# Optimization experiments

Measured on AMD Instinct MI355X. Metric: run time of the kernel, lower is better.

## Reference

```python
import jax, jax.numpy as jnp
import numpy as np

N_NODES = 20000
N_EDGES = 320000
IN_FEATS = 256
H_FEATS = 256


def setup_inputs() -> dict:
    key = jax.random.key(0)
    ks = jax.random.split(key, 8)
    s = 1.0 / np.sqrt(IN_FEATS)
    return {
        "features": jax.random.normal(ks[0], (N_NODES, IN_FEATS), jnp.float32),
        "src": jax.random.randint(ks[1], (N_EDGES,), 0, N_NODES, jnp.int32),
        "dst": jax.random.randint(ks[2], (N_EDGES,), 0, N_NODES, jnp.int32),
        "W_self1": jax.random.normal(ks[3], (IN_FEATS, H_FEATS), jnp.float32) * s,
        "W_neigh1": jax.random.normal(ks[4], (IN_FEATS, H_FEATS), jnp.float32) * s,
        "b1": jnp.zeros((H_FEATS,), jnp.float32),
        "W_self2": jax.random.normal(ks[5], (H_FEATS, H_FEATS), jnp.float32) * s,
        "W_neigh2": jax.random.normal(ks[6], (H_FEATS, H_FEATS), jnp.float32) * s,
        "b2": jnp.zeros((H_FEATS,), jnp.float32),
    }


def _sage_conv(h, src, dst, W_self, W_neigh, b, n_nodes):
    # mean aggregation of src features onto dst nodes (DGL SAGEConv 'mean')
    msg_sum = jax.ops.segment_sum(h[src], dst, num_segments=n_nodes)  # [N, d]
    deg = jax.ops.segment_sum(jnp.ones_like(dst, dtype=h.dtype), dst,
                              num_segments=n_nodes)  # [N]
    h_neigh = msg_sum / jnp.maximum(deg, 1.0)[:, None]  # isolated nodes -> 0
    return h @ W_self + h_neigh @ W_neigh + b


def reference(features, src, dst, W_self1, W_neigh1, b1, W_self2, W_neigh2, b2):
    n = features.shape[0]
    h = _sage_conv(features, src, dst, W_self1, W_neigh1, b1, n)
    h = jax.nn.relu(h)
    h = _sage_conv(h, src, dst, W_self2, W_neigh2, b2, n)
    # DotPredictor: per-edge dot product of src/dst embeddings
    score = jnp.sum(h[src] * h[dst], axis=1)  # [E]
    return score
```

## Files before the change

### kernel.cpp

```cpp
#include <hip/hip_runtime.h>
#include <hip/hip_bf16.h>
#include <stdint.h>

typedef __bf16 bf16_t;
typedef __bf16 bf16x8 __attribute__((ext_vector_type(8)));
typedef __bf16 bf16x4 __attribute__((ext_vector_type(4)));
typedef float f32x4 __attribute__((ext_vector_type(4)));

#define NFEAT 256
#define KDIM  512
#define BM 64
#define BN 128
#define BK 64

__device__ __forceinline__ void gload_lds16(const void* g, void* l) {
  __builtin_amdgcn_global_load_lds(
      (const __attribute__((address_space(1))) unsigned int*)g,
      (__attribute__((address_space(3))) unsigned int*)l, 16, 0, 0);
}


__global__ void k_count_deg(const int* __restrict__ dst, int* __restrict__ deg, int nE) {
  int i = blockIdx.x * blockDim.x + threadIdx.x;
  if (i < nE) atomicAdd(&deg[dst[i]], 1);
}

__global__ __launch_bounds__(256) void k_scan_part(const int* __restrict__ deg,
                                                   int* __restrict__ partial, int n) {
  const int tid = threadIdx.x;
  int i = blockIdx.x * 256 + tid;
  int d = (i < n) ? deg[i] : 0;
  #pragma unroll
  for (int off = 32; off; off >>= 1) d += __shfl_xor(d, off, 64);
  __shared__ int ws[4];
  if ((tid & 63) == 0) ws[tid >> 6] = d;
  __syncthreads();
  if (tid == 0) partial[blockIdx.x] = ws[0] + ws[1] + ws[2] + ws[3];
}

__global__ __launch_bounds__(256) void k_scan_final(const int* __restrict__ deg,
                                                    const int* __restrict__ partial,
                                                    int* __restrict__ offsets,
                                                    int* __restrict__ cursor,
                                                    float* __restrict__ inv_deg,
                                                    int n, int nb) {
  __shared__ int s[256], p[256];
  const int tid = threadIdx.x;
  int pv = (tid < nb) ? partial[tid] : 0;
  p[tid] = pv;
  __syncthreads();
  for (int off = 1; off < 256; off <<= 1) {
    int v = (tid >= off) ? p[tid - off] : 0;
    __syncthreads();
    p[tid] += v;
    __syncthreads();
  }
  int i = blockIdx.x * 256 + tid;
  int d = (i < n) ? deg[i] : 0;
  s[tid] = d;
  __syncthreads();
  for (int off = 1; off < 256; off <<= 1) {
    int v = (tid >= off) ? s[tid - off] : 0;
    __syncthreads();
    s[tid] += v;
    __syncthreads();
  }
  if (i < n) {
    int block_excl = p[blockIdx.x] - partial[blockIdx.x];
    int excl = block_excl + s[tid] - d;
    offsets[i] = excl;
    cursor[i]  = excl;
    inv_deg[i] = 1.0f / (float)(d > 1 ? d : 1);
  }
}

__global__ void k_scatter(const int* __restrict__ src, const int* __restrict__ dst,
                          int* __restrict__ cursor, int4* __restrict__ csr_pack, int nE) {
  int i = blockIdx.x * blockDim.x + threadIdx.x;
  if (i < nE) {
    int d = dst[i];
    int pos = atomicAdd(&cursor[d], 1);
    csr_pack[pos] = make_int4(src[i], d, i, 0);
  }
}

__global__ void k_prep(const float* __restrict__ F,
                       const float* __restrict__ Ws1, const float* __restrict__ Wn1,
                       const float* __restrict__ Ws2, const float* __restrict__ Wn2,
                       bf16_t* __restrict__ WT1, bf16_t* __restrict__ WT2,
                       bf16_t* __restrict__ X,
                       int* __restrict__ deg, int nNodes, int mpad) {
  int t = blockIdx.x * blockDim.x + threadIdx.x;
  if (t < mpad) deg[t] = 0;
  if (t < 2 * NFEAT * KDIM) {
    int layer = t >> 17;
    int r = t & (NFEAT * KDIM - 1);
    int n = r >> 9;
    int k = r & 511;
    const float* Ws = layer ? Ws2 : Ws1;
    const float* Wn = layer ? Wn2 : Wn1;
    float v = (k < NFEAT) ? Ws[k * NFEAT + n] : Wn[(k - NFEAT) * NFEAT + n];
    (layer ? WT2 : WT1)[r] = (bf16_t)v;
  }
  int n = t >> 6;
  int c = (t & 63) * 4;
  if (n < mpad) {
    float4 v = make_float4(0.f, 0.f, 0.f, 0.f);
    if (n < nNodes) v = *(const float4*)&F[(size_t)n * NFEAT + c];
    bf16x4 o;
    o[0] = (bf16_t)v.x; o[1] = (bf16_t)v.y; o[2] = (bf16_t)v.z; o[3] = (bf16_t)v.w;
    *(bf16x4*)&X[(size_t)n * KDIM + c] = o;
  }
}

__global__ __launch_bounds__(256) void k_agg(const bf16_t* __restrict__ Hin,
                                             bf16_t* __restrict__ Hout,
                                             const int4* __restrict__ csr_pack,
                                             const int* __restrict__ offsets,
                                             const int* __restrict__ deg,
                                             const float* __restrict__ inv_deg,
                                             int instride, int outstride) {
  const int n   = blockIdx.x * 8 + (threadIdx.x >> 5);
  const int l32 = threadIdx.x & 31;
  const int beg = offsets[n];
  const int cnt = deg[n];
  const size_t colo = (size_t)l32 * 8;

  float acc[8] = {0.f, 0.f, 0.f, 0.f, 0.f, 0.f, 0.f, 0.f};

  int s[4];
  #pragma unroll
  for (int q = 0; q < 4; ++q) s[q] = (q < cnt) ? csr_pack[beg + q].x : -1;

  for (int i = 0; i < cnt; i += 4) {
    bf16x8 v[4];
    bool h[4];
    #pragma unroll
    for (int q = 0; q < 4; ++q) {
      h[q] = (s[q] >= 0);
      if (h[q]) v[q] = *(const bf16x8*)&Hin[(size_t)s[q] * instride + colo];
    }
    #pragma unroll
    for (int q = 0; q < 4; ++q) {
      int j = i + 4 + q;
      s[q] = (j < cnt) ? csr_pack[beg + j].x : -1;
    }
    #pragma unroll
    for (int q = 0; q < 4; ++q) {
      if (h[q]) {
        #pragma unroll
        for (int e = 0; e < 8; ++e) acc[e] += (float)v[q][e];
      }
    }
  }

  float w = inv_deg[n];
  bf16x8 o;
  #pragma unroll
  for (int e = 0; e < 8; ++e) o[e] = (bf16_t)(acc[e] * w);
  *(bf16x8*)&Hout[(size_t)n * outstride + NFEAT + colo] = o;
}

__global__ __launch_bounds__(256, 3) void k_gemm(const bf16_t* __restrict__ A,
                                                 const bf16_t* __restrict__ BT,
                                                 const float* __restrict__ bias,
                                                 bf16_t* __restrict__ Cout,
                                                 int ostride, int relu) {
  __shared__ __align__(16) bf16_t As[2][BM * BK];
  __shared__ __align__(16) bf16_t Bs[2][BN * BK];
  const int tid  = threadIdx.x;
  const int lane = tid & 63;
  const int wave = tid >> 6;
  const int wr = wave >> 1, wc = wave & 1;
  const int m0 = blockIdx.x * BM;
  const int n0 = blockIdx.y * BN;
  const int l15 = lane & 15;
  const int lk8 = (lane >> 4) * 8;

  f32x4 acc[2][4] = {};

  auto stage = [&](int buf, int kt) {
    const int k0 = kt * BK;
    #pragma unroll
    for (int i = 0; i < 2; ++i) {
      int idx = i * 256 + tid;
      int row = idx >> 3;
      int c8  = (idx & 7) * 8;
      gload_lds16(A + (size_t)(m0 + row) * KDIM + k0 + c8,
                  (char*)&As[buf][0] + (i * 256 + wave * 64) * 16);
    }
    #pragma unroll
    for (int i = 0; i < 4; ++i) {
      int idx = i * 256 + tid;
      int row = idx >> 3;
      int c8  = (idx & 7) * 8;
      gload_lds16(BT + (size_t)(n0 + row) * KDIM + k0 + c8,
                  (char*)&Bs[buf][0] + (i * 256 + wave * 64) * 16);
    }
  };

  auto compute = [&](int buf) {
    #pragma unroll
    for (int kk = 0; kk < 2; ++kk) {
      bf16x8 af[2], bfr[4];
      #pragma unroll
      for (int m = 0; m < 2; ++m) {
        int row = wr * 32 + m * 16 + l15;
        af[m] = *(const bf16x8*)&As[buf][row * BK + kk * 32 + lk8];
      }
      #pragma unroll
      for (int n = 0; n < 4; ++n) {
        int col = wc * 64 + n * 16 + l15;
        bfr[n] = *(const bf16x8*)&Bs[buf][col * BK + kk * 32 + lk8];
      }
      #pragma unroll
      for (int m = 0; m < 2; ++m)
        #pragma unroll
        for (int n = 0; n < 4; ++n)
          acc[m][n] = __builtin_amdgcn_mfma_f32_16x16x32_bf16(af[m], bfr[n], acc[m][n], 0, 0, 0);
    }
  };

  stage(0, 0);
  __syncthreads();
  const int nt = KDIM / BK;
  int cur = 0;
  for (int t = 0; t < nt; ++t) {
    if (t + 1 < nt) stage(cur ^ 1, t + 1);
    compute(cur);
    __syncthreads();
    cur ^= 1;
  }

  #pragma unroll
  for (int n = 0; n < 4; ++n) {
    int col = n0 + wc * 64 + n * 16 + l15;
    float bv = bias[col];
    #pragma unroll
    for (int m = 0; m < 2; ++m) {
      int rbase = m0 + wr * 32 + m * 16 + (lane >> 4) * 4;
      #pragma unroll
      for (int j = 0; j < 4; ++j) {
        float v = acc[m][n][j] + bv;
        if (relu) v = fmaxf(v, 0.f);
        Cout[(size_t)(rbase + j) * ostride + col] = (bf16_t)v;
      }
    }
  }
}

__global__ __launch_bounds__(256) void k_edge_dot(const bf16_t* __restrict__ H,
                                                  const int4* __restrict__ csr_pack,
                                                  float* __restrict__ out, int nE) {
  const int wid  = (blockIdx.x * blockDim.x + threadIdx.x) >> 6;
  const int lane = threadIdx.x & 63;
  const int l15  = lane & 15;
  const int hi   = lane >> 4;
  const int e0   = wid * 16;
  if (e0 >= nE) return;
  int pos = e0 + l15;
  if (pos >= nE) pos = nE - 1;

  const int4 e = csr_pack[pos];
  const bf16_t* ps = H + (size_t)e.x * NFEAT + hi * 8;
  const bf16_t* pd = H + (size_t)e.y * NFEAT + hi * 8;

  f32x4 acc = {0.f, 0.f, 0.f, 0.f};
  #pragma unroll
  for (int ks = 0; ks < 8; ++ks) {
    bf16x8 a = *(const bf16x8*)(ps + ks * 32);
    bf16x8 b = *(const bf16x8*)(pd + ks * 32);
    acc = __builtin_amdgcn_mfma_f32_16x16x32_bf16(a, b, acc, 0, 0, 0);
  }

  if ((l15 >> 2) == hi && (e0 + l15) < nE) {
    int j = l15 & 3;
    float v = acc[0];
    v = (j == 1) ? acc[1] : v;
    v = (j == 2) ? acc[2] : v;
    v = (j == 3) ? acc[3] : v;
    out[e.z] = v;
  }
}


extern "C" void kernel_launch(void* const* d_in, const int* in_sizes, int n_in,
                              void* d_out, int out_size, void* d_ws, size_t ws_size,
                              hipStream_t stream) {
  const float* features = (const float*)d_in[0];
  const int*   src      = (const int*)d_in[1];
  const int*   dst      = (const int*)d_in[2];
  const float* Wself1   = (const float*)d_in[3];
  const float* Wneigh1  = (const float*)d_in[4];
  const float* b1       = (const float*)d_in[5];
  const float* Wself2   = (const float*)d_in[6];
  const float* Wneigh2  = (const float*)d_in[7];
  const float* b2       = (const float*)d_in[8];
  float* score = (float*)d_out;

  const int nNodes = in_sizes[0] / NFEAT;
  const int nE     = in_sizes[1];
  const int mpad   = ((nNodes + 127) / 128) * 128;

  char* ws = (char*)d_ws;
  size_t off = 0;
  auto alloc = [&](size_t bytes) { char* p = ws + off; off += (bytes + 255) & ~(size_t)255; return p; };
  bf16_t* Xcat1   = (bf16_t*)alloc((size_t)mpad * KDIM * 2);
  bf16_t* Xcat2   = (bf16_t*)alloc((size_t)mpad * KDIM * 2);
  bf16_t* H2      = (bf16_t*)alloc((size_t)mpad * NFEAT * 2);
  bf16_t* WT1     = (bf16_t*)alloc((size_t)NFEAT * KDIM * 2);
  bf16_t* WT2     = (bf16_t*)alloc((size_t)NFEAT * KDIM * 2);
  int*    deg     = (int*)alloc((size_t)mpad * 4);
  int*    offsets = (int*)alloc((size_t)mpad * 4);
  int*    cursor  = (int*)alloc((size_t)mpad * 4);
  float*  inv_deg = (float*)alloc((size_t)mpad * 4);
  int4*   csr_pack= (int4*)alloc((size_t)nE * 16);
  int*    partial = (int*)alloc(1024 * 4);

  const int eb = (nE + 255) / 256;
  const int nb = (mpad + 255) / 256;

  k_prep<<<(mpad * 64 + 255) / 256, 256, 0, stream>>>(features, Wself1, Wneigh1,
                                                      Wself2, Wneigh2, WT1, WT2,
                                                      Xcat1, deg, nNodes, mpad);

  k_count_deg<<<eb, 256, 0, stream>>>(dst, deg, nE);
  k_scan_part<<<nb, 256, 0, stream>>>(deg, partial, mpad);
  k_scan_final<<<nb, 256, 0, stream>>>(deg, partial, offsets, cursor, inv_deg, mpad, nb);
  k_scatter<<<eb, 256, 0, stream>>>(src, dst, cursor, csr_pack, nE);

  k_agg<<<mpad / 8, 256, 0, stream>>>(Xcat1, Xcat1, csr_pack, offsets, deg, inv_deg, KDIM, KDIM);
  dim3 ggrid(mpad / BM, NFEAT / BN);
  k_gemm<<<ggrid, 256, 0, stream>>>(Xcat1, WT1, b1, Xcat2, KDIM, 1);

  k_agg<<<mpad / 8, 256, 0, stream>>>(Xcat2, Xcat2, csr_pack, offsets, deg, inv_deg, KDIM, KDIM);
  k_gemm<<<ggrid, 256, 0, stream>>>(Xcat2, WT2, b2, H2, NFEAT, 0);

  const int nWaves = (nE + 15) / 16;
  k_edge_dot<<<(nWaves + 3) / 4, 256, 0, stream>>>(H2, csr_pack, score, nE);
}
```

Baseline: 152.1 us.

## Fuse neighbor aggregation into GEMM, single-pass scan, and compact CSR edge packing

Mean aggregation now runs inside the GEMM kernel. Each block gathers neighbor rows for its 64 nodes into a swizzled LDS tile and uses that tile as the second half of K, so the aggregated features no longer go through global memory and the separate agg launches are dropped. The GEMM tile widens to the full 256 output columns with 512 threads. The two scan kernels become one decoupled-lookback scan that spins on global flags and resets them for the next call. The CSR pack shrinks from int4 to a src array plus an int2 holding 16-bit-packed src/dst and the edge id. The 16-bit packing assumes fewer than 65536 nodes, the spin-wait relies on all blocks making forward progress, and the fused kernel needs much more LDS, which may lower occupancy.

```diff
diff --git a/kernel.cpp b/kernel.cpp
--- a/kernel.cpp
+++ b/kernel.cpp
@@ -10,7 +10,7 @@
 #define NFEAT 256
 #define KDIM  512
 #define BM 64
-#define BN 128
+#define BN 256
 #define BK 64
 
 __device__ __forceinline__ void gload_lds16(const void* g, void* l) {
@@ -19,43 +19,25 @@
       (__attribute__((address_space(3))) unsigned int*)l, 16, 0, 0);
 }
 
+__device__ int g_flag[256];
+__device__ int g_depart;
+
 
 __global__ void k_count_deg(const int* __restrict__ dst, int* __restrict__ deg, int nE) {
   int i = blockIdx.x * blockDim.x + threadIdx.x;
   if (i < nE) atomicAdd(&deg[dst[i]], 1);
 }
 
-__global__ __launch_bounds__(256) void k_scan_part(const int* __restrict__ deg,
-                                                   int* __restrict__ partial, int n) {
-  const int tid = threadIdx.x;
-  int i = blockIdx.x * 256 + tid;
-  int d = (i < n) ? deg[i] : 0;
-  #pragma unroll
-  for (int off = 32; off; off >>= 1) d += __shfl_xor(d, off, 64);
-  __shared__ int ws[4];
-  if ((tid & 63) == 0) ws[tid >> 6] = d;
-  __syncthreads();
-  if (tid == 0) partial[blockIdx.x] = ws[0] + ws[1] + ws[2] + ws[3];
-}
-
-__global__ __launch_bounds__(256) void k_scan_final(const int* __restrict__ deg,
-                                                    const int* __restrict__ partial,
+__global__ __launch_bounds__(256) void k_scan_fused(const int* __restrict__ deg,
                                                     int* __restrict__ offsets,
                                                     int* __restrict__ cursor,
                                                     float* __restrict__ inv_deg,
                                                     int n, int nb) {
-  __shared__ int s[256], p[256];
+  __shared__ int s[256];
+  __shared__ int p[256];
+  const int b = blockIdx.x;
   const int tid = threadIdx.x;
-  int pv = (tid < nb) ? partial[tid] : 0;
-  p[tid] = pv;
-  __syncthreads();
-  for (int off = 1; off < 256; off <<= 1) {
-    int v = (tid >= off) ? p[tid - off] : 0;
-    __syncthreads();
-    p[tid] += v;
-    __syncthreads();
-  }
-  int i = blockIdx.x * 256 + tid;
+  int i = b * 256 + tid;
   int d = (i < n) ? deg[i] : 0;
   s[tid] = d;
   __syncthreads();
@@ -65,22 +47,46 @@
     s[tid] += v;
     __syncthreads();
   }
+  if (tid == 255) atomicExch(&g_flag[b], s[255] + 1);
+  int pv = 0;
+  if (tid < b) {
+    int v;
+    do { v = atomicAdd(&g_flag[tid], 0); } while (v == 0);
+    pv = v - 1;
+  }
+  p[tid] = pv;
+  __syncthreads();
+  for (int off = 128; off; off >>= 1) {
+    if (tid < off) p[tid] += p[tid + off];
+    __syncthreads();
+  }
+  int block_excl = p[0];
   if (i < n) {
-    int block_excl = p[blockIdx.x] - partial[blockIdx.x];
     int excl = block_excl + s[tid] - d;
     offsets[i] = excl;
     cursor[i]  = excl;
     inv_deg[i] = 1.0f / (float)(d > 1 ? d : 1);
   }
+  __syncthreads();
+  if (tid == 0) {
+    int old = atomicAdd(&g_depart, 1);
+    if (old == nb - 1) {
+      for (int j = 0; j < nb; ++j) atomicExch(&g_flag[j], 0);
+      atomicExch(&g_depart, 0);
+    }
+  }
 }
 
 __global__ void k_scatter(const int* __restrict__ src, const int* __restrict__ dst,
-                          int* __restrict__ cursor, int4* __restrict__ csr_pack, int nE) {
+                          int* __restrict__ cursor, int* __restrict__ csr_src,
+                          int2* __restrict__ epack, int nE) {
   int i = blockIdx.x * blockDim.x + threadIdx.x;
   if (i < nE) {
     int d = dst[i];
+    int s = src[i];
     int pos = atomicAdd(&cursor[d], 1);
-    csr_pack[pos] = make_int4(src[i], d, i, 0);
+    csr_src[pos] = s;
+    epack[pos] = make_int2((d << 16) | s, i);
   }
 }
 
@@ -109,148 +115,152 @@
     if (n < nNodes) v = *(const float4*)&F[(size_t)n * NFEAT + c];
     bf16x4 o;
     o[0] = (bf16_t)v.x; o[1] = (bf16_t)v.y; o[2] = (bf16_t)v.z; o[3] = (bf16_t)v.w;
-    *(bf16x4*)&X[(size_t)n * KDIM + c] = o;
-  }
-}
-
-__global__ __launch_bounds__(256) void k_agg(const bf16_t* __restrict__ Hin,
-                                             bf16_t* __restrict__ Hout,
-                                             const int4* __restrict__ csr_pack,
-                                             const int* __restrict__ offsets,
-                                             const int* __restrict__ deg,
-                                             const float* __restrict__ inv_deg,
-                                             int instride, int outstride) {
-  const int n   = blockIdx.x * 8 + (threadIdx.x >> 5);
-  const int l32 = threadIdx.x & 31;
-  const int beg = offsets[n];
-  const int cnt = deg[n];
-  const size_t colo = (size_t)l32 * 8;
-
-  float acc[8] = {0.f, 0.f, 0.f, 0.f, 0.f, 0.f, 0.f, 0.f};
-
-  int s[4];
-  #pragma unroll
-  for (int q = 0; q < 4; ++q) s[q] = (q < cnt) ? csr_pack[beg + q].x : -1;
-
-  for (int i = 0; i < cnt; i += 4) {
-    bf16x8 v[4];
-    bool h[4];
-    #pragma unroll
-    for (int q = 0; q < 4; ++q) {
-      h[q] = (s[q] >= 0);
-      if (h[q]) v[q] = *(const bf16x8*)&Hin[(size_t)s[q] * instride + colo];
-    }
-    #pragma unroll
-    for (int q = 0; q < 4; ++q) {
-      int j = i + 4 + q;
-      s[q] = (j < cnt) ? csr_pack[beg + j].x : -1;
-    }
-    #pragma unroll
-    for (int q = 0; q < 4; ++q) {
-      if (h[q]) {
-        #pragma unroll
-        for (int e = 0; e < 8; ++e) acc[e] += (float)v[q][e];
-      }
-    }
-  }
-
-  float w = inv_deg[n];
-  bf16x8 o;
-  #pragma unroll
-  for (int e = 0; e < 8; ++e) o[e] = (bf16_t)(acc[e] * w);
-  *(bf16x8*)&Hout[(size_t)n * outstride + NFEAT + colo] = o;
-}
-
-__global__ __launch_bounds__(256, 3) void k_gemm(const bf16_t* __restrict__ A,
-                                                 const bf16_t* __restrict__ BT,
-                                                 const float* __restrict__ bias,
-                                                 bf16_t* __restrict__ Cout,
-                                                 int ostride, int relu) {
+    *(bf16x4*)&X[(size_t)n * NFEAT + c] = o;
+  }
+}
+
+__global__ __launch_bounds__(512, 2) void k_gemm_agg(
+    const bf16_t* __restrict__ Xin,
+    const bf16_t* __restrict__ BT,
+    const float*  __restrict__ bias,
+    bf16_t* __restrict__ Cout,
+    const int* __restrict__ csr_src,
+    const int* __restrict__ offsets,
+    const int* __restrict__ deg,
+    const float* __restrict__ inv_deg,
+    int relu) {
   __shared__ __align__(16) bf16_t As[2][BM * BK];
   __shared__ __align__(16) bf16_t Bs[2][BN * BK];
+  __shared__ __align__(16) bf16_t Ag[BM * 256];
   const int tid  = threadIdx.x;
   const int lane = tid & 63;
   const int wave = tid >> 6;
-  const int wr = wave >> 1, wc = wave & 1;
-  const int m0 = blockIdx.x * BM;
-  const int n0 = blockIdx.y * BN;
-  const int l15 = lane & 15;
-  const int lk8 = (lane >> 4) * 8;
-
-  f32x4 acc[2][4] = {};
-
-  auto stage = [&](int buf, int kt) {
-    const int k0 = kt * BK;
+  const int wr   = wave >> 2;
+  const int wc   = wave & 3;
+  const int m0   = blockIdx.x * BM;
+  const int l15  = lane & 15;
+  const int hi4  = lane >> 4;
+  const int lk8  = hi4 * 8;
+
+  auto stageA = [&](int buf, int kt) {
+    int row = tid >> 3;
+    int c8  = (tid & 7) * 8;
+    gload_lds16(Xin + (size_t)(m0 + row) * NFEAT + kt * BK + c8,
+                (char*)&As[buf][0] + wave * 1024);
+  };
+  auto stageB = [&](int buf, int kt) {
     #pragma unroll
-    for (int i = 0; i < 2; ++i) {
-      int idx = i * 256 + tid;
+    for (int i = 0; i < 4; ++i) {
+      int idx = i * 512 + tid;
       int row = idx >> 3;
       int c8  = (idx & 7) * 8;
-      gload_lds16(A + (size_t)(m0 + row) * KDIM + k0 + c8,
-                  (char*)&As[buf][0] + (i * 256 + wave * 64) * 16);
-    }
-    #pragma unroll
-    for (int i = 0; i < 4; ++i) {
-      int idx = i * 256 + tid;
-      int row = idx >> 3;
-      int c8  = (idx & 7) * 8;
-      gload_lds16(BT + (size_t)(n0 + row) * KDIM + k0 + c8,
-                  (char*)&Bs[buf][0] + (i * 256 + wave * 64) * 16);
+      gload_lds16(BT + (size_t)row * KDIM + kt * BK + c8,
+                  (char*)&Bs[buf][0] + (i * 512 + wave * 64) * 16);
     }
   };
 
-  auto compute = [&](int buf) {
+  stageA(0, 0);
+  stageB(0, 0);
+
+  {
+    const int hw  = tid >> 5;
+    const int l32 = tid & 31;
+    const size_t colo = (size_t)l32 * 8;
+    for (int r = 0; r < 4; ++r) {
+      const int n   = m0 + hw * 4 + r;
+      const int beg = offsets[n];
+      const int cnt = deg[n];
+      float acc[8] = {0.f, 0.f, 0.f, 0.f, 0.f, 0.f, 0.f, 0.f};
+      int sq[4];
+      #pragma unroll
+      for (int q = 0; q < 4; ++q) sq[q] = (q < cnt) ? csr_src[beg + q] : -1;
+      for (int i = 0; i < cnt; i += 4) {
+        bf16x8 v[4];
+        bool h[4];
+        #pragma unroll
+        for (int q = 0; q < 4; ++q) {
+          h[q] = (sq[q] >= 0);
+          if (h[q]) v[q] = *(const bf16x8*)&Xin[(size_t)sq[q] * NFEAT + colo];
+        }
+        #pragma unroll
+        for (int q = 0; q < 4; ++q) {
+          int j = i + 4 + q;
+          sq[q] = (j < cnt) ? csr_src[beg + j] : -1;
+        }
+        #pragma unroll
+        for (int q = 0; q < 4; ++q) {
+          if (h[q]) {
+            #pragma unroll
+            for (int e = 0; e < 8; ++e) acc[e] += (float)v[q][e];
+          }
+        }
+      }
+      float w = inv_deg[n];
+      bf16x8 o;
+      #pragma unroll
+      for (int e = 0; e < 8; ++e) o[e] = (bf16_t)(acc[e] * w);
+      const int row = hw * 4 + r;
+      const int byteo = row * 512 + ((l32 * 16) ^ ((row & 7) << 4));
+      *(bf16x8*)((char*)Ag + byteo) = o;
+    }
+  }
+  __syncthreads();
+
+  f32x4 acc[2][4] = {};
+  int cur = 0;
+  #pragma unroll
+  for (int t = 0; t < 8; ++t) {
+    if (t < 7) {
+      if (t + 1 < 4) stageA(cur ^ 1, t + 1);
+      stageB(cur ^ 1, t + 1);
+    }
     #pragma unroll
     for (int kk = 0; kk < 2; ++kk) {
       bf16x8 af[2], bfr[4];
       #pragma unroll
       for (int m = 0; m < 2; ++m) {
-        int row = wr * 32 + m * 16 + l15;
-        af[m] = *(const bf16x8*)&As[buf][row * BK + kk * 32 + lk8];
+        const int row = wr * 32 + m * 16 + l15;
+        if (t < 4) {
+          af[m] = *(const bf16x8*)&As[cur][row * BK + kk * 32 + lk8];
+        } else {
+          const int cb = (t - 4) * 128 + kk * 64 + hi4 * 16;
+          af[m] = *(const bf16x8*)((char*)Ag + row * 512 + (cb ^ ((row & 7) << 4)));
+        }
       }
       #pragma unroll
-      for (int n = 0; n < 4; ++n) {
-        int col = wc * 64 + n * 16 + l15;
-        bfr[n] = *(const bf16x8*)&Bs[buf][col * BK + kk * 32 + lk8];
+      for (int nn = 0; nn < 4; ++nn) {
+        const int col = wc * 64 + nn * 16 + l15;
+        bfr[nn] = *(const bf16x8*)&Bs[cur][col * BK + kk * 32 + lk8];
       }
       #pragma unroll
       for (int m = 0; m < 2; ++m)
         #pragma unroll
-        for (int n = 0; n < 4; ++n)
-          acc[m][n] = __builtin_amdgcn_mfma_f32_16x16x32_bf16(af[m], bfr[n], acc[m][n], 0, 0, 0);
-    }
-  };
-
-  stage(0, 0);
-  __syncthreads();
-  const int nt = KDIM / BK;
-  int cur = 0;
-  for (int t = 0; t < nt; ++t) {
-    if (t + 1 < nt) stage(cur ^ 1, t + 1);
-    compute(cur);
+        for (int nn = 0; nn < 4; ++nn)
+          acc[m][nn] = __builtin_amdgcn_mfma_f32_16x16x32_bf16(af[m], bfr[nn], acc[m][nn], 0, 0, 0);
+    }
     __syncthreads();
     cur ^= 1;
   }
 
   #pragma unroll
-  for (int n = 0; n < 4; ++n) {
-    int col = n0 + wc * 64 + n * 16 + l15;
-    float bv = bias[col];
+  for (int nn = 0; nn < 4; ++nn) {
+    const int col = wc * 64 + nn * 16 + l15;
+    const float bv = bias[col];
     #pragma unroll
     for (int m = 0; m < 2; ++m) {
-      int rbase = m0 + wr * 32 + m * 16 + (lane >> 4) * 4;
+      const int rbase = m0 + wr * 32 + m * 16 + hi4 * 4;
       #pragma unroll
       for (int j = 0; j < 4; ++j) {
-        float v = acc[m][n][j] + bv;
+        float v = acc[m][nn][j] + bv;
         if (relu) v = fmaxf(v, 0.f);
-        Cout[(size_t)(rbase + j) * ostride + col] = (bf16_t)v;
+        Cout[(size_t)(rbase + j) * NFEAT + col] = (bf16_t)v;
       }
     }
   }
 }
 
 __global__ __launch_bounds__(256) void k_edge_dot(const bf16_t* __restrict__ H,
-                                                  const int4* __restrict__ csr_pack,
+                                                  const int2* __restrict__ epack,
                                                   float* __restrict__ out, int nE) {
   const int wid  = (blockIdx.x * blockDim.x + threadIdx.x) >> 6;
   const int lane = threadIdx.x & 63;
@@ -261,9 +271,11 @@
   int pos = e0 + l15;
   if (pos >= nE) pos = nE - 1;
 
-  const int4 e = csr_pack[pos];
-  const bf16_t* ps = H + (size_t)e.x * NFEAT + hi * 8;
-  const bf16_t* pd = H + (size_t)e.y * NFEAT + hi * 8;
+  const int2 e = epack[pos];
+  const int s = e.x & 0xFFFF;
+  const int d = ((unsigned)e.x) >> 16;
+  const bf16_t* ps = H + (size_t)s * NFEAT + hi * 8;
+  const bf16_t* pd = H + (size_t)d * NFEAT + hi * 8;
 
   f32x4 acc = {0.f, 0.f, 0.f, 0.f};
   #pragma unroll
@@ -279,7 +291,7 @@
     v = (j == 1) ? acc[1] : v;
     v = (j == 2) ? acc[2] : v;
     v = (j == 3) ? acc[3] : v;
-    out[e.z] = v;
+    out[e.y] = v;
   }
 }
 
@@ -305,8 +317,8 @@
   char* ws = (char*)d_ws;
   size_t off = 0;
   auto alloc = [&](size_t bytes) { char* p = ws + off; off += (bytes + 255) & ~(size_t)255; return p; };
-  bf16_t* Xcat1   = (bf16_t*)alloc((size_t)mpad * KDIM * 2);
-  bf16_t* Xcat2   = (bf16_t*)alloc((size_t)mpad * KDIM * 2);
+  bf16_t* Xcat1   = (bf16_t*)alloc((size_t)mpad * NFEAT * 2);
+  bf16_t* Xcat2   = (bf16_t*)alloc((size_t)mpad * NFEAT * 2);
   bf16_t* H2      = (bf16_t*)alloc((size_t)mpad * NFEAT * 2);
   bf16_t* WT1     = (bf16_t*)alloc((size_t)NFEAT * KDIM * 2);
   bf16_t* WT2     = (bf16_t*)alloc((size_t)NFEAT * KDIM * 2);
@@ -314,8 +326,8 @@
   int*    offsets = (int*)alloc((size_t)mpad * 4);
   int*    cursor  = (int*)alloc((size_t)mpad * 4);
   float*  inv_deg = (float*)alloc((size_t)mpad * 4);
-  int4*   csr_pack= (int4*)alloc((size_t)nE * 16);
-  int*    partial = (int*)alloc(1024 * 4);
+  int*    csr_src = (int*)alloc((size_t)nE * 4);
+  int2*   epack   = (int2*)alloc((size_t)nE * 8);
 
   const int eb = (nE + 255) / 256;
   const int nb = (mpad + 255) / 256;
@@ -325,17 +337,14 @@
                                                       Xcat1, deg, nNodes, mpad);
 
   k_count_deg<<<eb, 256, 0, stream>>>(dst, deg, nE);
-  k_scan_part<<<nb, 256, 0, stream>>>(deg, partial, mpad);
-  k_scan_final<<<nb, 256, 0, stream>>>(deg, partial, offsets, cursor, inv_deg, mpad, nb);
-  k_scatter<<<eb, 256, 0, stream>>>(src, dst, cursor, csr_pack, nE);
-
-  k_agg<<<mpad / 8, 256, 0, stream>>>(Xcat1, Xcat1, csr_pack, offsets, deg, inv_deg, KDIM, KDIM);
-  dim3 ggrid(mpad / BM, NFEAT / BN);
-  k_gemm<<<ggrid, 256, 0, stream>>>(Xcat1, WT1, b1, Xcat2, KDIM, 1);
-
-  k_agg<<<mpad / 8, 256, 0, stream>>>(Xcat2, Xcat2, csr_pack, offsets, deg, inv_deg, KDIM, KDIM);
-  k_gemm<<<ggrid, 256, 0, stream>>>(Xcat2, WT2, b2, H2, NFEAT, 0);
+  k_scan_fused<<<nb, 256, 0, stream>>>(deg, offsets, cursor, inv_deg, mpad, nb);
+  k_scatter<<<eb, 256, 0, stream>>>(src, dst, cursor, csr_src, epack, nE);
+
+  k_gemm_agg<<<mpad / BM, 512, 0, stream>>>(Xcat1, WT1, b1, Xcat2,
+                                            csr_src, offsets, deg, inv_deg, 1);
+  k_gemm_agg<<<mpad / BM, 512, 0, stream>>>(Xcat2, WT2, b2, H2,
+                                            csr_src, offsets, deg, inv_deg, 0);
 
   const int nWaves = (nE + 15) / 16;
-  k_edge_dot<<<(nWaves + 3) / 4, 256, 0, stream>>>(H2, csr_pack, score, nE);
-}
+  k_edge_dot<<<(nWaves + 3) / 4, 256, 0, stream>>>(H2, epack, score, nE);
+}
```

Result: slower. 193.9 us (+27.4%).

## Fuse scan passes with decoupled lookback and split CSR into compact arrays

Applied to the files above, without the earlier changes.

Replaces the two-kernel prefix scan with a single kernel in which each block publishes its total through a global flag array and sums its predecessors' totals, resetting the flags at the end for the next call. The 16-byte CSR edge record is split into a 4-byte source array for aggregation and an 8-byte pack holding src and dst as 16-bit fields plus the edge id, used by the edge-dot kernel. This removes one launch and reduces index bandwidth in aggregation and edge scoring. It depends on all scan blocks being co-resident to avoid deadlock, and on node ids fitting in 16 bits.

```diff
diff --git a/kernel.cpp b/kernel.cpp
--- a/kernel.cpp
+++ b/kernel.cpp
@@ -19,43 +19,25 @@
       (__attribute__((address_space(3))) unsigned int*)l, 16, 0, 0);
 }
 
+__device__ int g_flag[256];
+__device__ int g_depart;
+
 
 __global__ void k_count_deg(const int* __restrict__ dst, int* __restrict__ deg, int nE) {
   int i = blockIdx.x * blockDim.x + threadIdx.x;
   if (i < nE) atomicAdd(&deg[dst[i]], 1);
 }
 
-__global__ __launch_bounds__(256) void k_scan_part(const int* __restrict__ deg,
-                                                   int* __restrict__ partial, int n) {
-  const int tid = threadIdx.x;
-  int i = blockIdx.x * 256 + tid;
-  int d = (i < n) ? deg[i] : 0;
-  #pragma unroll
-  for (int off = 32; off; off >>= 1) d += __shfl_xor(d, off, 64);
-  __shared__ int ws[4];
-  if ((tid & 63) == 0) ws[tid >> 6] = d;
-  __syncthreads();
-  if (tid == 0) partial[blockIdx.x] = ws[0] + ws[1] + ws[2] + ws[3];
-}
-
-__global__ __launch_bounds__(256) void k_scan_final(const int* __restrict__ deg,
-                                                    const int* __restrict__ partial,
+__global__ __launch_bounds__(256) void k_scan_fused(const int* __restrict__ deg,
                                                     int* __restrict__ offsets,
                                                     int* __restrict__ cursor,
                                                     float* __restrict__ inv_deg,
                                                     int n, int nb) {
-  __shared__ int s[256], p[256];
+  __shared__ int s[256];
+  __shared__ int p[256];
+  const int b = blockIdx.x;
   const int tid = threadIdx.x;
-  int pv = (tid < nb) ? partial[tid] : 0;
-  p[tid] = pv;
-  __syncthreads();
-  for (int off = 1; off < 256; off <<= 1) {
-    int v = (tid >= off) ? p[tid - off] : 0;
-    __syncthreads();
-    p[tid] += v;
-    __syncthreads();
-  }
-  int i = blockIdx.x * 256 + tid;
+  int i = b * 256 + tid;
   int d = (i < n) ? deg[i] : 0;
   s[tid] = d;
   __syncthreads();
@@ -65,22 +47,46 @@
     s[tid] += v;
     __syncthreads();
   }
+  if (tid == 255) atomicExch(&g_flag[b], s[255] + 1);
+  int pv = 0;
+  if (tid < b) {
+    int v;
+    do { v = atomicAdd(&g_flag[tid], 0); } while (v == 0);
+    pv = v - 1;
+  }
+  p[tid] = pv;
+  __syncthreads();
+  for (int off = 128; off; off >>= 1) {
+    if (tid < off) p[tid] += p[tid + off];
+    __syncthreads();
+  }
+  int block_excl = p[0];
   if (i < n) {
-    int block_excl = p[blockIdx.x] - partial[blockIdx.x];
     int excl = block_excl + s[tid] - d;
     offsets[i] = excl;
     cursor[i]  = excl;
     inv_deg[i] = 1.0f / (float)(d > 1 ? d : 1);
   }
+  __syncthreads();
+  if (tid == 0) {
+    int old = atomicAdd(&g_depart, 1);
+    if (old == nb - 1) {
+      for (int j = 0; j < nb; ++j) atomicExch(&g_flag[j], 0);
+      atomicExch(&g_depart, 0);
+    }
+  }
 }
 
 __global__ void k_scatter(const int* __restrict__ src, const int* __restrict__ dst,
-                          int* __restrict__ cursor, int4* __restrict__ csr_pack, int nE) {
+                          int* __restrict__ cursor, int* __restrict__ csr_src,
+                          int2* __restrict__ epack, int nE) {
   int i = blockIdx.x * blockDim.x + threadIdx.x;
   if (i < nE) {
     int d = dst[i];
+    int s = src[i];
     int pos = atomicAdd(&cursor[d], 1);
-    csr_pack[pos] = make_int4(src[i], d, i, 0);
+    csr_src[pos] = s;
+    epack[pos] = make_int2((d << 16) | s, i);
   }
 }
 
@@ -115,7 +121,7 @@
 
 __global__ __launch_bounds__(256) void k_agg(const bf16_t* __restrict__ Hin,
                                              bf16_t* __restrict__ Hout,
-                                             const int4* __restrict__ csr_pack,
+                                             const int* __restrict__ csr_src,
                                              const int* __restrict__ offsets,
                                              const int* __restrict__ deg,
                                              const float* __restrict__ inv_deg,
@@ -130,7 +136,7 @@
 
   int s[4];
   #pragma unroll
-  for (int q = 0; q < 4; ++q) s[q] = (q < cnt) ? csr_pack[beg + q].x : -1;
+  for (int q = 0; q < 4; ++q) s[q] = (q < cnt) ? csr_src[beg + q] : -1;
 
   for (int i = 0; i < cnt; i += 4) {
     bf16x8 v[4];
@@ -143,7 +149,7 @@
     #pragma unroll
     for (int q = 0; q < 4; ++q) {
       int j = i + 4 + q;
-      s[q] = (j < cnt) ? csr_pack[beg + j].x : -1;
+      s[q] = (j < cnt) ? csr_src[beg + j] : -1;
     }
     #pragma unroll
     for (int q = 0; q < 4; ++q) {
@@ -250,7 +256,7 @@
 }
 
 __global__ __launch_bounds__(256) void k_edge_dot(const bf16_t* __restrict__ H,
-                                                  const int4* __restrict__ csr_pack,
+                                                  const int2* __restrict__ epack,
                                                   float* __restrict__ out, int nE) {
   const int wid  = (blockIdx.x * blockDim.x + threadIdx.x) >> 6;
   const int lane = threadIdx.x & 63;
@@ -261,9 +267,11 @@
   int pos = e0 + l15;
   if (pos >= nE) pos = nE - 1;
 
-  const int4 e = csr_pack[pos];
-  const bf16_t* ps = H + (size_t)e.x * NFEAT + hi * 8;
-  const bf16_t* pd = H + (size_t)e.y * NFEAT + hi * 8;
+  const int2 e = epack[pos];
+  const int s = e.x & 0xFFFF;
+  const int d = ((unsigned)e.x) >> 16;
+  const bf16_t* ps = H + (size_t)s * NFEAT + hi * 8;
+  const bf16_t* pd = H + (size_t)d * NFEAT + hi * 8;
 
   f32x4 acc = {0.f, 0.f, 0.f, 0.f};
   #pragma unroll
@@ -279,7 +287,7 @@
     v = (j == 1) ? acc[1] : v;
     v = (j == 2) ? acc[2] : v;
     v = (j == 3) ? acc[3] : v;
-    out[e.z] = v;
+    out[e.y] = v;
   }
 }
 
@@ -314,8 +322,8 @@
   int*    offsets = (int*)alloc((size_t)mpad * 4);
   int*    cursor  = (int*)alloc((size_t)mpad * 4);
   float*  inv_deg = (float*)alloc((size_t)mpad * 4);
-  int4*   csr_pack= (int4*)alloc((size_t)nE * 16);
-  int*    partial = (int*)alloc(1024 * 4);
+  int*    csr_src = (int*)alloc((size_t)nE * 4);
+  int2*   epack   = (int2*)alloc((size_t)nE * 8);
 
   const int eb = (nE + 255) / 256;
   const int nb = (mpad + 255) / 256;
@@ -325,17 +333,16 @@
                                                       Xcat1, deg, nNodes, mpad);
 
   k_count_deg<<<eb, 256, 0, stream>>>(dst, deg, nE);
-  k_scan_part<<<nb, 256, 0, stream>>>(deg, partial, mpad);
-  k_scan_final<<<nb, 256, 0, stream>>>(deg, partial, offsets, cursor, inv_deg, mpad, nb);
-  k_scatter<<<eb, 256, 0, stream>>>(src, dst, cursor, csr_pack, nE);
-
-  k_agg<<<mpad / 8, 256, 0, stream>>>(Xcat1, Xcat1, csr_pack, offsets, deg, inv_deg, KDIM, KDIM);
+  k_scan_fused<<<nb, 256, 0, stream>>>(deg, offsets, cursor, inv_deg, mpad, nb);
+  k_scatter<<<eb, 256, 0, stream>>>(src, dst, cursor, csr_src, epack, nE);
+
+  k_agg<<<mpad / 8, 256, 0, stream>>>(Xcat1, Xcat1, csr_src, offsets, deg, inv_deg, KDIM, KDIM);
   dim3 ggrid(mpad / BM, NFEAT / BN);
   k_gemm<<<ggrid, 256, 0, stream>>>(Xcat1, WT1, b1, Xcat2, KDIM, 1);
 
-  k_agg<<<mpad / 8, 256, 0, stream>>>(Xcat2, Xcat2, csr_pack, offsets, deg, inv_deg, KDIM, KDIM);
+  k_agg<<<mpad / 8, 256, 0, stream>>>(Xcat2, Xcat2, csr_src, offsets, deg, inv_deg, KDIM, KDIM);
   k_gemm<<<ggrid, 256, 0, stream>>>(Xcat2, WT2, b2, H2, NFEAT, 0);
 
   const int nWaves = (nE + 15) / 16;
-  k_edge_dot<<<(nWaves + 3) / 4, 256, 0, stream>>>(H2, csr_pack, score, nE);
-}
+  k_edge_dot<<<(nWaves + 3) / 4, 256, 0, stream>>>(H2, epack, score, nE);
+}
```

Measured after the change: 155.8 us. +2.4%, slower.
